# Kernel optimization log

Hardware: AMD Instinct MI355X
Metric: run time of the kernel (lower is better)

The kernel has to match this reference:

```python
import jax, jax.numpy as jnp
import numpy as np
from jax import lax

SIGMA = 1.0
ALPHA = 1.0
BETA = 1.0
TRUNCATE = 4.0  # scipy.ndimage default


def _gauss_kernel(sigma):
    radius = int(TRUNCATE * sigma + 0.5)  # scipy radius rule -> 4 for sigma=1
    x = np.arange(-radius, radius + 1, dtype=np.float64)
    k = np.exp(-0.5 * (x / sigma) ** 2)
    k = (k / k.sum()).astype(np.float32)
    return k

_KERNEL = _gauss_kernel(SIGMA)


def _blur_axis(img, k, axis):
    # scipy mode='reflect' == jnp.pad mode='symmetric' (edge repeated)
    r = len(k) // 2
    pad = [(0, 0)] * img.ndim
    pad[axis] = (r, r)
    xp = jnp.pad(img, pad, mode='symmetric')
    n = img.shape[axis]
    out = k[0] * lax.slice_in_dim(xp, 0, n, axis=axis)
    for i in range(1, len(k)):
        out = out + k[i] * lax.slice_in_dim(xp, i, i + n, axis=axis)
    return out


def gaussian_blur(img):
    # scalar sigma in scipy blurs along EVERY axis, including batch & channel
    k = jnp.asarray(_KERNEL, dtype=img.dtype)
    for ax in range(img.ndim):
        img = _blur_axis(img, k, ax)
    return img


def decompose(I):
    I_log = jnp.log(I + 1e-6)
    I_smooth = gaussian_blur(I_log)
    R = I_log - I_smooth
    L = I_log - R  # == I_smooth
    return jnp.exp(L), jnp.exp(R)


def setup_inputs() -> dict:
    key = jax.random.key(0)
    k1, k2 = jax.random.split(key)
    shape = (16, 3, 512, 512)
    I_enhanced = jax.random.uniform(k1, shape, dtype=jnp.float32)
    I_gt = jax.random.uniform(k2, shape, dtype=jnp.float32)
    return {"I_enhanced": I_enhanced, "I_gt": I_gt}


def reference(I_enhanced, I_gt):
    L_enh, R_enh = decompose(I_enhanced)
    L_gt, R_gt = decompose(I_gt)
    L_reflectance = jnp.mean((R_enh - R_gt) ** 2)
    L_illumination = jnp.mean((L_enh - L_gt) ** 2)
    return ALPHA * L_reflectance + BETA * L_illumination
```

## Files before the change

kernel.cpp:

```cpp
#include <hip/hip_runtime.h>
#include <cmath>

#define PLANE (512*512)
#define NPLANES 48
#define NEL (48*PLANE)

struct Taps  { float k[9]; };
struct CMat  { float w[3][3]; };

__global__ __launch_bounds__(256)
void k_blur_hw(const float* __restrict__ inE, const float* __restrict__ inG,
               float* __restrict__ outE, float* __restrict__ outG, Taps tp)
{
    __shared__ float raw[72*72];
    __shared__ float wb[72*64];

    const int tid = threadIdx.x;
    const int w0 = blockIdx.x * 64;
    const int h0 = blockIdx.y * 64;
    const int z  = blockIdx.z;

    const float* src;
    float* dst;
    if (z < NPLANES) { src = inE + z * PLANE;              dst = outE + z * PLANE; }
    else             { src = inG + (z - NPLANES) * PLANE;  dst = outG + (z - NPLANES) * PLANE; }

    for (int j = tid; j < 72*72; j += 256) {
        int r = j / 72;
        int c = j - r * 72;
        int h = h0 + r - 4; h = (h < 0) ? (-1 - h) : ((h > 511) ? (1023 - h) : h);
        int w = w0 + c - 4; w = (w < 0) ? (-1 - w) : ((w > 511) ? (1023 - w) : w);
        raw[j] = __logf(src[h * 512 + w] + 1e-6f);
    }
    __syncthreads();

    for (int j = tid; j < 72*16; j += 256) {
        int r  = j >> 4;
        int cg = (j & 15) << 2;
        const float4* rp = (const float4*)&raw[r * 72 + cg];
        float x[12];
        ((float4*)x)[0] = rp[0];
        ((float4*)x)[1] = rp[1];
        ((float4*)x)[2] = rp[2];
        float4 o = make_float4(0.f, 0.f, 0.f, 0.f);
#pragma unroll
        for (int t = 0; t < 9; ++t) {
            float kt = tp.k[t];
            o.x += kt * x[t];
            o.y += kt * x[t + 1];
            o.z += kt * x[t + 2];
            o.w += kt * x[t + 3];
        }
        *(float4*)&wb[r * 64 + cg] = o;
    }
    __syncthreads();

    for (int j = tid; j < 1024; j += 256) {
        int c  = j & 63;
        int rb = (j >> 6) << 2;
        float x[12];
#pragma unroll
        for (int t = 0; t < 12; ++t) x[t] = wb[(rb + t) * 64 + c];
#pragma unroll
        for (int i = 0; i < 4; ++i) {
            float s = 0.f;
#pragma unroll
            for (int t = 0; t < 9; ++t) s += tp.k[t] * x[i + t];
            dst[(h0 + rb + i) * 512 + (w0 + c)] = s;
        }
    }
}

__global__ __launch_bounds__(256)
void k_cn_loss(const float* __restrict__ Ae, const float* __restrict__ Ag,
               const float* __restrict__ Ie, const float* __restrict__ Ig,
               float* __restrict__ part, Taps tp, CMat cm)
{
    const int hw = blockIdx.x * 256 + threadIdx.x;

    float re[9][3];
    float rg[9][3];

#define LOADCB(m, ring, A)                                                    \
    {                                                                         \
        float v0 = A[((m) * 3 + 0) * PLANE + hw];                             \
        float v1 = A[((m) * 3 + 1) * PLANE + hw];                             \
        float v2 = A[((m) * 3 + 2) * PLANE + hw];                             \
        ring[(m) % 9][0] = cm.w[0][0] * v0 + cm.w[0][1] * v1 + cm.w[0][2] * v2; \
        ring[(m) % 9][1] = cm.w[1][0] * v0 + cm.w[1][1] * v1 + cm.w[1][2] * v2; \
        ring[(m) % 9][2] = cm.w[2][0] * v0 + cm.w[2][1] * v1 + cm.w[2][2] * v2; \
    }

#pragma unroll
    for (int m = 0; m < 4; ++m) { LOADCB(m, re, Ae); LOADCB(m, rg, Ag); }

    float acc = 0.f;
#pragma unroll
    for (int n = 0; n < 16; ++n) {
        const int mnew = n + 4;
        if (mnew < 16) { LOADCB(mnew, re, Ae); LOADCB(mnew, rg, Ag); }
#pragma unroll
        for (int c = 0; c < 3; ++c) {
            float se = 0.f, sg = 0.f;
#pragma unroll
            for (int t = 0; t < 9; ++t) {
                int m = n - 4 + t;
                m = (m < 0) ? (-1 - m) : ((m > 15) ? (31 - m) : m);
                se += tp.k[t] * re[m % 9][c];
                sg += tp.k[t] * rg[m % 9][c];
            }
            const int j = n * 3 + c;
            float ie = Ie[j * PLANE + hw] + 1e-6f;
            float ig = Ig[j * PLANE + hw] + 1e-6f;
            float ee = __expf(-se);
            float eg = __expf(-sg);
            float Re = ie * ee;
            float Rg = ig * eg;
            float Le = __builtin_amdgcn_rcpf(ee);
            float Lg = __builtin_amdgcn_rcpf(eg);
            float dr = Re - Rg;
            float dl = Le - Lg;
            acc += dr * dr + dl * dl;
        }
    }
#undef LOADCB

    __shared__ float red[256];
    red[threadIdx.x] = acc;
    __syncthreads();
#pragma unroll
    for (int s = 128; s > 0; s >>= 1) {
        if (threadIdx.x < s) red[threadIdx.x] += red[threadIdx.x + s];
        __syncthreads();
    }
    if (threadIdx.x == 0) part[blockIdx.x] = red[0];
}

__global__ __launch_bounds__(256)
void k_final(const float* __restrict__ part, float* __restrict__ out)
{
    __shared__ float red[256];
    float a = 0.f;
    for (int i = threadIdx.x; i < 1024; i += 256) a += part[i];
    red[threadIdx.x] = a;
    __syncthreads();
#pragma unroll
    for (int s = 128; s > 0; s >>= 1) {
        if (threadIdx.x < s) red[threadIdx.x] += red[threadIdx.x + s];
        __syncthreads();
    }
    if (threadIdx.x == 0) out[0] = red[0] * (1.0f / (float)NEL);
}

extern "C" void kernel_launch(void* const* d_in, const int* in_sizes, int n_in,
                              void* d_out, int out_size, void* d_ws, size_t ws_size,
                              hipStream_t stream) {
    const float* Ie = (const float*)d_in[0];
    const float* Ig = (const float*)d_in[1];

    Taps tp;
    {
        double kk[9], s = 0.0;
        for (int i = 0; i < 9; ++i) { double x = (double)(i - 4); kk[i] = exp(-0.5 * x * x); s += kk[i]; }
        for (int i = 0; i < 9; ++i) tp.k[i] = (float)(kk[i] / s);
    }

    CMat cm;
    {
        for (int c = 0; c < 3; ++c) {
            cm.w[c][0] = cm.w[c][1] = cm.w[c][2] = 0.f;
            for (int t = 0; t < 9; ++t) {
                int m = c - 4 + t;
                int mm = ((m % 6) + 6) % 6;
                if (mm > 2) mm = 5 - mm;
                cm.w[c][mm] += tp.k[t];
            }
        }
    }

    float* Ae   = (float*)d_ws;
    float* Ag   = Ae + NEL;
    float* part = Ag + NEL;

    dim3 g1(8, 8, 96);
    k_blur_hw<<<g1, 256, 0, stream>>>(Ie, Ig, Ae, Ag, tp);
    k_cn_loss<<<1024, 256, 0, stream>>>(Ae, Ag, Ie, Ig, part, tp, cm);
    k_final<<<1, 256, 0, stream>>>(part, (float*)d_out);
}
```

Baseline: 190.1 us.

## Rewrite HW blur as register-streaming wavefront with interleaved plane layout

Replaces the shared-memory tiled 2D blur with a one-wavefront-per-32-row-strip kernel. Each lane owns 8 columns of a full 512-wide row, gets the horizontal halo through lane shuffles, and keeps a 10-row register ring for the vertical pass, which removes LDS staging and the redundant halo loads and log evaluations. The intermediate is written in an interleaved layout with all 96 planes adjacent per 64-pixel group, so the channel/batch loss kernel reads neighbouring planes from nearby addresses. The cost is a small grid (1536 single-wave blocks) with heavy register use, which may limit latency hiding, and the store pattern is strided across planes.

```diff
diff --git a/kernel.cpp b/kernel.cpp
--- a/kernel.cpp
+++ b/kernel.cpp
@@ -5,100 +5,121 @@
 #define NPLANES 48
 #define NEL (48*PLANE)
 
-struct Taps  { float k[9]; };
-struct CMat  { float w[3][3]; };
+struct Taps { float k[9]; };
+struct CMat { float w[3][3]; };
+
+
+__global__ __launch_bounds__(64)
+void k_blur_hw(const float* __restrict__ inE, const float* __restrict__ inG,
+               float* __restrict__ ws, Taps tp)
+{
+    const int l  = threadIdx.x;
+    const int r0 = blockIdx.x * 32;
+    const int z  = blockIdx.y;
+
+    const float* src = (z < NPLANES) ? (inE + z * PLANE)
+                                     : (inG + (z - NPLANES) * PLANE);
+
+    const bool is0  = (l == 0);
+    const bool is63 = (l == 63);
+    const int  vout = (l >> 3) * 6144 + (l & 7) * 8;
+
+    float ring[10][8];
+
+    int rp0 = r0 - 4;
+    rp0 = (rp0 < 0) ? (-1 - rp0) : ((rp0 > 511) ? (1023 - rp0) : rp0);
+    float4 a = *(const float4*)(src + rp0 * 512 + l * 8);
+    float4 b = *(const float4*)(src + rp0 * 512 + l * 8 + 4);
+
+    for (int jb = 0; jb < 40; jb += 10) {
+#pragma unroll
+        for (int u = 0; u < 10; ++u) {
+            const int j = jb + u;
+
+            int rn = r0 - 4 + j + 1;
+            rn = (rn < 0) ? (-1 - rn) : ((rn > 511) ? (1023 - rn) : rn);
+            const float* nrp = src + rn * 512 + l * 8;
+            float4 na = *(const float4*)nrp;
+            float4 nb = *(const float4*)(nrp + 4);
+
+            float win[16];
+            win[4]  = __logf(a.x + 1e-6f);
+            win[5]  = __logf(a.y + 1e-6f);
+            win[6]  = __logf(a.z + 1e-6f);
+            win[7]  = __logf(a.w + 1e-6f);
+            win[8]  = __logf(b.x + 1e-6f);
+            win[9]  = __logf(b.y + 1e-6f);
+            win[10] = __logf(b.z + 1e-6f);
+            win[11] = __logf(b.w + 1e-6f);
+
+            float s;
+            s = __shfl_up(win[8], 1);   win[0]  = is0  ? win[7]  : s;
+            s = __shfl_up(win[9], 1);   win[1]  = is0  ? win[6]  : s;
+            s = __shfl_up(win[10], 1);  win[2]  = is0  ? win[5]  : s;
+            s = __shfl_up(win[11], 1);  win[3]  = is0  ? win[4]  : s;
+            s = __shfl_down(win[4], 1); win[12] = is63 ? win[11] : s;
+            s = __shfl_down(win[5], 1); win[13] = is63 ? win[10] : s;
+            s = __shfl_down(win[6], 1); win[14] = is63 ? win[9]  : s;
+            s = __shfl_down(win[7], 1); win[15] = is63 ? win[8]  : s;
+
+#pragma unroll
+            for (int i = 0; i < 8; ++i) {
+                float o = 0.f;
+#pragma unroll
+                for (int t = 0; t < 9; ++t) o += tp.k[t] * win[i + t];
+                ring[u][i] = o;
+            }
+
+            if (j >= 8) {
+                float acc[8];
+#pragma unroll
+                for (int i = 0; i < 8; ++i) {
+                    float o = 0.f;
+#pragma unroll
+                    for (int t = 0; t < 9; ++t)
+                        o += tp.k[t] * ring[(u + 2 + t) % 10][i];
+                    acc[i] = o;
+                }
+                const int ro = r0 + j - 8;
+                float* dp = ws + (ro * 768 + z) * 64 + vout;
+                *(float4*)dp       = make_float4(acc[0], acc[1], acc[2], acc[3]);
+                *(float4*)(dp + 4) = make_float4(acc[4], acc[5], acc[6], acc[7]);
+            }
+            a = na; b = nb;
+        }
+    }
+}
 
 __global__ __launch_bounds__(256)
-void k_blur_hw(const float* __restrict__ inE, const float* __restrict__ inG,
-               float* __restrict__ outE, float* __restrict__ outG, Taps tp)
+void k_cn_loss(const float* __restrict__ ws, const float* __restrict__ Ie,
+               const float* __restrict__ Ig, float* __restrict__ part,
+               Taps tp, CMat cm)
 {
-    __shared__ float raw[72*72];
-    __shared__ float wb[72*64];
-
     const int tid = threadIdx.x;
-    const int w0 = blockIdx.x * 64;
-    const int h0 = blockIdx.y * 64;
-    const int z  = blockIdx.z;
-
-    const float* src;
-    float* dst;
-    if (z < NPLANES) { src = inE + z * PLANE;              dst = outE + z * PLANE; }
-    else             { src = inG + (z - NPLANES) * PLANE;  dst = outG + (z - NPLANES) * PLANE; }
-
-    for (int j = tid; j < 72*72; j += 256) {
-        int r = j / 72;
-        int c = j - r * 72;
-        int h = h0 + r - 4; h = (h < 0) ? (-1 - h) : ((h > 511) ? (1023 - h) : h);
-        int w = w0 + c - 4; w = (w < 0) ? (-1 - w) : ((w > 511) ? (1023 - w) : w);
-        raw[j] = __logf(src[h * 512 + w] + 1e-6f);
-    }
-    __syncthreads();
-
-    for (int j = tid; j < 72*16; j += 256) {
-        int r  = j >> 4;
-        int cg = (j & 15) << 2;
-        const float4* rp = (const float4*)&raw[r * 72 + cg];
-        float x[12];
-        ((float4*)x)[0] = rp[0];
-        ((float4*)x)[1] = rp[1];
-        ((float4*)x)[2] = rp[2];
-        float4 o = make_float4(0.f, 0.f, 0.f, 0.f);
-#pragma unroll
-        for (int t = 0; t < 9; ++t) {
-            float kt = tp.k[t];
-            o.x += kt * x[t];
-            o.y += kt * x[t + 1];
-            o.z += kt * x[t + 2];
-            o.w += kt * x[t + 3];
-        }
-        *(float4*)&wb[r * 64 + cg] = o;
-    }
-    __syncthreads();
-
-    for (int j = tid; j < 1024; j += 256) {
-        int c  = j & 63;
-        int rb = (j >> 6) << 2;
-        float x[12];
-#pragma unroll
-        for (int t = 0; t < 12; ++t) x[t] = wb[(rb + t) * 64 + c];
-#pragma unroll
-        for (int i = 0; i < 4; ++i) {
-            float s = 0.f;
-#pragma unroll
-            for (int t = 0; t < 9; ++t) s += tp.k[t] * x[i + t];
-            dst[(h0 + rb + i) * 512 + (w0 + c)] = s;
-        }
-    }
-}
-
-__global__ __launch_bounds__(256)
-void k_cn_loss(const float* __restrict__ Ae, const float* __restrict__ Ag,
-               const float* __restrict__ Ie, const float* __restrict__ Ig,
-               float* __restrict__ part, Taps tp, CMat cm)
-{
-    const int hw = blockIdx.x * 256 + threadIdx.x;
+    const int hw  = blockIdx.x * 256 + tid;
+    const float* wbase = ws + (hw >> 6) * (96 * 64) + (hw & 63);
 
     float re[9][3];
     float rg[9][3];
 
-#define LOADCB(m, ring, A)                                                    \
-    {                                                                         \
-        float v0 = A[((m) * 3 + 0) * PLANE + hw];                             \
-        float v1 = A[((m) * 3 + 1) * PLANE + hw];                             \
-        float v2 = A[((m) * 3 + 2) * PLANE + hw];                             \
-        ring[(m) % 9][0] = cm.w[0][0] * v0 + cm.w[0][1] * v1 + cm.w[0][2] * v2; \
-        ring[(m) % 9][1] = cm.w[1][0] * v0 + cm.w[1][1] * v1 + cm.w[1][2] * v2; \
-        ring[(m) % 9][2] = cm.w[2][0] * v0 + cm.w[2][1] * v1 + cm.w[2][2] * v2; \
-    }
-
-#pragma unroll
-    for (int m = 0; m < 4; ++m) { LOADCB(m, re, Ae); LOADCB(m, rg, Ag); }
+#define LOADCB(m, ring, OFF)                                                   \
+    {                                                                          \
+        float v0 = wbase[((OFF) + (m) * 3 + 0) * 64];                          \
+        float v1 = wbase[((OFF) + (m) * 3 + 1) * 64];                          \
+        float v2 = wbase[((OFF) + (m) * 3 + 2) * 64];                          \
+        ring[(m) % 9][0] = cm.w[0][0]*v0 + cm.w[0][1]*v1 + cm.w[0][2]*v2;      \
+        ring[(m) % 9][1] = cm.w[1][0]*v0 + cm.w[1][1]*v1 + cm.w[1][2]*v2;      \
+        ring[(m) % 9][2] = cm.w[2][0]*v0 + cm.w[2][1]*v1 + cm.w[2][2]*v2;      \
+    }
+
+#pragma unroll
+    for (int m = 0; m < 4; ++m) { LOADCB(m, re, 0); LOADCB(m, rg, 48); }
 
     float acc = 0.f;
 #pragma unroll
     for (int n = 0; n < 16; ++n) {
         const int mnew = n + 4;
-        if (mnew < 16) { LOADCB(mnew, re, Ae); LOADCB(mnew, rg, Ag); }
+        if (mnew < 16) { LOADCB(mnew, re, 0); LOADCB(mnew, rg, 48); }
 #pragma unroll
         for (int c = 0; c < 3; ++c) {
             float se = 0.f, sg = 0.f;
@@ -126,14 +147,14 @@
 #undef LOADCB
 
     __shared__ float red[256];
-    red[threadIdx.x] = acc;
+    red[tid] = acc;
     __syncthreads();
 #pragma unroll
     for (int s = 128; s > 0; s >>= 1) {
-        if (threadIdx.x < s) red[threadIdx.x] += red[threadIdx.x + s];
+        if (tid < s) red[tid] += red[tid + s];
         __syncthreads();
     }
-    if (threadIdx.x == 0) part[blockIdx.x] = red[0];
+    if (tid == 0) part[blockIdx.x] = red[0];
 }
 
 __global__ __launch_bounds__(256)
@@ -178,12 +199,11 @@
         }
     }
 
-    float* Ae   = (float*)d_ws;
-    float* Ag   = Ae + NEL;
-    float* part = Ag + NEL;
-
-    dim3 g1(8, 8, 96);
-    k_blur_hw<<<g1, 256, 0, stream>>>(Ie, Ig, Ae, Ag, tp);
-    k_cn_loss<<<1024, 256, 0, stream>>>(Ae, Ag, Ie, Ig, part, tp, cm);
+    float* ws   = (float*)d_ws;
+    float* part = ws + 2 * (size_t)NEL;
+
+    dim3 g1(16, 96);
+    k_blur_hw<<<g1, 64, 0, stream>>>(Ie, Ig, ws, tp);
+    k_cn_loss<<<1024, 256, 0, stream>>>(ws, Ie, Ig, part, tp, cm);
     k_final<<<1, 256, 0, stream>>>(part, (float*)d_out);
 }
```

Result: faster. 181.7 us (-4.4%).
